# Performance work log

Hardware: AMD Instinct MI355X
Metric: run time of the kernel (lower is better)

Reference implementation:

```python
import jax, jax.numpy as jnp
import numpy as np

LMAX = 3
L2 = (LMAX + 1) ** 2
EPS = 1e-5
N_NODES = 2048
C_IN = 384
C_HID = 256


def _gaunt_tensor(lmax):
    # Real Gaunt coefficients G[i,j,k] = integral Y_i Y_j Y_k dOmega over S^2,
    # computed exactly with Gauss-Legendre (theta) x uniform (phi) quadrature.
    nt = 4 * lmax + 4
    nph = 8 * lmax + 8
    xg, wg = np.polynomial.legendre.leggauss(nt)
    ct, st = xg, np.sqrt(1.0 - xg ** 2)
    phi = 2.0 * np.pi * np.arange(nph) / nph
    # fully-normalized associated Legendre Pbar[l,m] on theta nodes
    P = np.zeros((lmax + 1, lmax + 1, nt))
    P[0, 0] = np.sqrt(1.0 / (4.0 * np.pi))
    for m in range(1, lmax + 1):
        P[m, m] = np.sqrt((2.0 * m + 1.0) / (2.0 * m)) * st * P[m - 1, m - 1]
    for m in range(lmax + 1):
        if m + 1 <= lmax:
            P[m + 1, m] = np.sqrt(2.0 * m + 3.0) * ct * P[m, m]
        for l in range(m + 2, lmax + 1):
            a = np.sqrt((4.0 * l * l - 1.0) / (l * l - m * m))
            b = np.sqrt(((l - 1.0) ** 2 - m * m) / (4.0 * (l - 1.0) ** 2 - 1.0))
            P[l, m] = a * (ct * P[l - 1, m] - b * P[l - 2, m])
    Y = np.zeros(((lmax + 1) ** 2, nt, nph))
    for l in range(lmax + 1):
        for m in range(-l, l + 1):
            idx = l * l + l + m
            if m == 0:
                Y[idx] = P[l, 0][:, None] * np.ones((1, nph))
            elif m > 0:
                Y[idx] = np.sqrt(2.0) * P[l, m][:, None] * np.cos(m * phi)[None, :]
            else:
                Y[idx] = np.sqrt(2.0) * P[l, -m][:, None] * np.sin(-m * phi)[None, :]
    W = wg[:, None] * (2.0 * np.pi / nph)  # [nt, nph]
    G = np.einsum('iap,jap,kap->ijk', Y, Y, Y * W[None])
    G[np.abs(G) < 1e-10] = 0.0
    return G


G_NP = _gaunt_tensor(LMAX)
SL = [slice(l * l, (l + 1) * (l + 1)) for l in range(LMAX + 1)]
_raw = []
for _l1 in range(LMAX + 1):
    for _l2 in range(LMAX + 1):
        for _l3 in range(LMAX + 1):
            _blk = G_NP[SL[_l1], SL[_l2], SL[_l3]]
            if np.abs(_blk).max() > 1e-8:
                _raw.append((_l1, _l2, _l3, _blk))
_fanin = {}
for _l1, _l2, _l3, _b in _raw:
    _fanin[_l3] = _fanin.get(_l3, 0) + 1
# component irrep normalization (sqrt(2l3+1)) and path normalization (1/sqrt(fan-in))
PATHS = [(l1, l2, l3, jnp.asarray((blk * np.sqrt(2.0 * l3 + 1.0) / np.sqrt(_fanin[l3])).astype(np.float32)))
         for (l1, l2, l3, blk) in _raw]
L_OF = jnp.asarray(np.repeat(np.arange(LMAX + 1), 2 * np.arange(LMAX + 1) + 1))  # [L2]


def setup_inputs() -> dict:
    key = jax.random.key(0)
    ks = jax.random.split(key, 9)
    inputs = jax.random.normal(ks[0], (N_NODES, L2, C_IN), jnp.float32)
    batch = jnp.sort(jax.random.randint(ks[1], (N_NODES,), 0, 64))
    norm_w = 1.0 + 0.1 * jax.random.normal(ks[2], (LMAX + 1, C_IN), jnp.float32)
    norm_b = 0.02 * jax.random.normal(ks[3], (C_IN,), jnp.float32)
    w1 = jax.random.normal(ks[4], (LMAX + 1, C_IN, C_HID), jnp.float32) / np.sqrt(C_IN)
    b1 = 0.02 * jax.random.normal(ks[5], (C_HID,), jnp.float32)
    w_gaunt = jax.random.normal(ks[6], (LMAX + 1, LMAX + 1, LMAX + 1, C_HID), jnp.float32)
    w2 = jax.random.normal(ks[7], (LMAX + 1, C_HID, C_IN), jnp.float32) / np.sqrt(C_HID)
    b2 = 0.02 * jax.random.normal(ks[8], (C_IN,), jnp.float32)
    return {"inputs": inputs, "batch": batch, "norm_w": norm_w, "norm_b": norm_b,
            "w1": w1, "b1": b1, "w_gaunt": w_gaunt, "w2": w2, "b2": b2}


def _forward(inputs, norm_w, norm_b, w1, b1, w_gaunt, w2, b2):
    # equivariant merge layer norm: center l=0 over channels, RMS over all (lm, C),
    # per-degree affine weight, bias on the l=0 (invariant) component only
    x = inputs
    x = x.at[:, 0, :].add(-jnp.mean(x[:, 0, :], axis=-1, keepdims=True))
    x = x * jax.lax.rsqrt(jnp.mean(x * x, axis=(1, 2), keepdims=True) + EPS)
    x = x * norm_w[L_OF][None]          # [N, L2, C]
    x = x.at[:, 0, :].add(norm_b)
    # SO3Linear 1: per-degree channel mixing, bias on l=0
    h = jnp.einsum('nic,ich->nih', x, w1[L_OF])
    h = h.at[:, 0, :].add(b1)
    # Gaunt depthwise self tensor product: per-channel CG-structured contraction
    t = jnp.zeros((inputs.shape[0], L2, w1.shape[-1]), dtype=h.dtype)
    for (l1, l2, l3, blk) in PATHS:
        hw = h[:, SL[l2], :] * w_gaunt[l1, l2, l3][None, None, :]     # [N, 2l2+1, H]
        tmp = jnp.einsum('ijk,nih->njkh', blk, h[:, SL[l1], :])       # small block contraction
        t = t.at[:, SL[l3], :].add(jnp.einsum('njkh,njh->nkh', tmp, hw))
    # SO3Linear 2
    out = jnp.einsum('nih,iho->nio', t, w2[L_OF])
    out = out.at[:, 0, :].add(b2)
    return out + inputs  # ffn_shortcut is Identity (num_in == num_out)


def reference(inputs, batch, norm_w, norm_b, w1, b1, w_gaunt, w2, b2):
    # drop_path / proj_drop are disabled (rates = 0); `batch` only feeds GraphDropPath
    return _forward(inputs, norm_w, norm_b, w1, b1, w_gaunt, w2, b2)
```

## Files before the change

kernel.cpp:

```cpp
#include <hip/hip_runtime.h>
#include <stdint.h>
#include <math.h>
#include <array>
#include <utility>

#ifndef M_PI
#define M_PI 3.14159265358979323846
#endif

#define NNODES 2048
#define L2DIM  16
#define CIN    384
#define CHID   256

typedef __attribute__((ext_vector_type(8))) short short8;
typedef __attribute__((ext_vector_type(4))) float f32x4;
typedef unsigned short u16;
typedef unsigned int   u32;

#define LOF(i) ((i) < 1 ? 0 : ((i) < 4 ? 1 : ((i) < 9 ? 2 : 3)))

static __device__ __forceinline__ u16 f2bf(float f) {
  u32 u = __builtin_bit_cast(u32, f);
  u = u + 0x7FFFu + ((u >> 16) & 1u);
  return (u16)(u >> 16);
}
static __device__ __forceinline__ float bf2f(u16 b) {
  u32 u = ((u32)b) << 16;
  return __builtin_bit_cast(float, u);
}

constexpr double CPI = 3.14159265358979323846;

constexpr double csqrt(double x) {
  if (x <= 0.0) return 0.0;
  double y = x > 1.0 ? x : 1.0;
  for (int i = 0; i < 48; ++i) y = 0.5 * (y + x / y);
  return y;
}
constexpr double ccos(double x) {
  double r = x;
  while (r > CPI)  r -= 2.0 * CPI;
  while (r < -CPI) r += 2.0 * CPI;
  double r2 = r * r, term = 1.0, sum = 1.0;
  for (int i = 1; i <= 26; ++i) { term *= -r2 / ((2.0 * i - 1.0) * (2.0 * i)); sum += term; }
  return sum;
}
constexpr int iabs_c(int x) { return x < 0 ? -x : x; }

struct GLQ { double x[16]; double w[16]; };
constexpr GLQ build_gl() {
  GLQ g{};
  const int n = 16;
  for (int i = 0; i < n; ++i) {
    double x = ccos(CPI * (i + 0.75) / (n + 0.5));
    double p1 = 0.0, dp = 1.0;
    for (int it = 0; it < 40; ++it) {
      double p0 = 1.0; p1 = x;
      for (int k = 2; k <= n; ++k) { double p2 = ((2.0*k-1.0)*x*p1 - (k-1.0)*p0)/k; p0 = p1; p1 = p2; }
      dp = n * (x*p1 - p0) / (x*x - 1.0);
      x -= p1 / dp;
    }
    { double p0 = 1.0; p1 = x;
      for (int k = 2; k <= n; ++k) { double p2 = ((2.0*k-1.0)*x*p1 - (k-1.0)*p0)/k; p0 = p1; p1 = p2; }
      dp = n * (x*p1 - p0) / (x*x - 1.0); }
    g.x[i] = x;
    g.w[i] = 2.0 / ((1.0 - x*x) * dp * dp);
  }
  return g;
}
constexpr GLQ QG = build_gl();

struct PTab { double v[4][4][16]; };
constexpr PTab build_pbar() {
  PTab T{};
  for (int t = 0; t < 16; ++t) {
    double ct = QG.x[t];
    double st = csqrt(1.0 - ct * ct);
    double P[4][4] = {};
    P[0][0] = csqrt(1.0 / (4.0 * CPI));
    for (int m = 1; m <= 3; ++m)
      P[m][m] = csqrt((2.0*m + 1.0) / (2.0*m)) * st * P[m-1][m-1];
    for (int m = 0; m <= 3; ++m) {
      if (m + 1 <= 3) P[m+1][m] = csqrt(2.0*m + 3.0) * ct * P[m][m];
      for (int l = m + 2; l <= 3; ++l) {
        double aa = csqrt((4.0*(double)l*l - 1.0) / ((double)l*l - (double)m*m));
        double bb = csqrt(((double)(l-1)*(l-1) - (double)m*m) / (4.0*(double)(l-1)*(l-1) - 1.0));
        P[l][m] = aa * (ct * P[l-1][m] - bb * P[l-2][m]);
      }
    }
    for (int l = 0; l < 4; ++l)
      for (int m = 0; m <= l; ++m) T.v[l][m][t] = P[l][m];
  }
  return T;
}
constexpr PTab PT = build_pbar();

constexpr double phi_int(int m1, int m2, int m3) {
  const double SQ2 = 1.41421356237309504880;
  int neg = (m1 < 0) + (m2 < 0) + (m3 < 0);
  if (neg & 1) return 0.0;
  int a = iabs_c(m1), b = iabs_c(m2), c = iabs_c(m3);
  int nz = (a > 0) + (b > 0) + (c > 0);
  if (nz == 0) return 2.0 * CPI;
  if (nz == 1) return 0.0;
  if (nz == 2) {
    int p = 0, q = 0;
    if (a == 0) { p = b; q = c; } else if (b == 0) { p = a; q = c; } else { p = a; q = b; }
    return (p == q) ? 2.0 * CPI : 0.0;
  }
  if (neg == 0) {
    double v = 0.0;
    if (iabs_c(a - b) == c && a != b) v += 1.0;
    if (a + b == c) v += 1.0;
    return SQ2 * CPI * v;
  }
  int p, q, r;
  if (m1 > 0)      { p = a; q = b; r = c; }
  else if (m2 > 0) { p = b; q = a; r = c; }
  else             { p = c; q = a; r = b; }
  double v = 0.0;
  if (q != r && p == iabs_c(q - r)) v += 1.0;
  if (p == q + r) v -= 1.0;
  return SQ2 * CPI * v;
}

constexpr bool path_ok(int l1, int l2, int l3) {
  int lo = l1 > l2 ? l1 - l2 : l2 - l1;
  return l3 >= lo && l3 <= l1 + l2 && (((l1 + l2 + l3) & 1) == 0);
}
constexpr bool term_ok(int m1, int m2, int m3) {
  int aa = iabs_c(m1), bb = iabs_c(m2), cc = iabs_c(m3);
  int neg = (m1 < 0) + (m2 < 0) + (m3 < 0);
  if (neg & 1) return false;
  return (aa + bb == cc) || (bb + cc == aa) || (cc + aa == bb);
}
constexpr int count_paths() {
  int n = 0;
  for (int l1 = 0; l1 < 4; ++l1) for (int l2 = 0; l2 < 4; ++l2) for (int l3 = 0; l3 < 4; ++l3)
    if (path_ok(l1, l2, l3)) ++n;
  return n;
}
constexpr int NPATHS = count_paths();
constexpr int NTMAX  = 512;

constexpr double term_g(int l1, int m1, int l2, int m2, int l3, int m3) {
  double ph = phi_int(m1, m2, m3);
  if (ph == 0.0) return 0.0;
  int a = iabs_c(m1), b = iabs_c(m2), c = iabs_c(m3);
  double s = 0.0;
  for (int t = 0; t < 16; ++t)
    s += QG.w[t] * PT.v[l1][a][t] * PT.v[l2][b][t] * PT.v[l3][c][t];
  double g = ph * s;
  double fan = (l3 == 0) ? 4.0 : (l3 == 1 ? 6.0 : (l3 == 2 ? 7.0 : 6.0));
  return g * csqrt((2.0 * (double)l3 + 1.0) / fan);
}

struct TermG { float g; unsigned char i, j, k, p; };
struct PathT { unsigned char l1, l2, l3; };
struct TGAll { TermG t[NTMAX]; int n; };
constexpr TGAll build_all() {
  TGAll r{};
  r.n = 0;
  int p = 0;
  for (int l1 = 0; l1 < 4; ++l1) for (int l2 = 0; l2 < 4; ++l2) for (int l3 = 0; l3 < 4; ++l3) {
    if (!path_ok(l1, l2, l3)) continue;
    for (int m1 = -l1; m1 <= l1; ++m1) for (int m2 = -l2; m2 <= l2; ++m2) for (int m3 = -l3; m3 <= l3; ++m3) {
      if (!term_ok(m1, m2, m3)) continue;
      double g = term_g(l1, m1, l2, m2, l3, m3);
      if (g > 1e-10 || g < -1e-10) {
        r.t[r.n].g = (float)g;
        r.t[r.n].i = (unsigned char)(l1 * l1 + l1 + m1);
        r.t[r.n].j = (unsigned char)(l2 * l2 + l2 + m2);
        r.t[r.n].k = (unsigned char)(l3 * l3 + l3 + m3);
        r.t[r.n].p = (unsigned char)p;
        ++r.n;
      }
    }
    ++p;
  }
  return r;
}
constexpr TGAll TGA = build_all();
constexpr int NNZ = TGA.n;

constexpr std::array<PathT, NPATHS> build_paths() {
  std::array<PathT, NPATHS> a{};
  int n = 0;
  for (int l1 = 0; l1 < 4; ++l1) for (int l2 = 0; l2 < 4; ++l2) for (int l3 = 0; l3 < 4; ++l3)
    if (path_ok(l1, l2, l3)) a[n++] = PathT{(unsigned char)l1, (unsigned char)l2, (unsigned char)l3};
  return a;
}
constexpr auto PATHS_ARR = build_paths();

template <size_t... Is>
__device__ __forceinline__ void gaunt_terms(std::index_sequence<Is...>,
    float* __restrict__ t, const float* __restrict__ h,
    const float* __restrict__ wgv) {
  ((t[TGA.t[Is].k] = fmaf(TGA.t[Is].g * wgv[TGA.t[Is].p],
                          h[TGA.t[Is].i] * h[TGA.t[Is].j],
                          t[TGA.t[Is].k])), ...);
}
template <size_t... Ps>
__device__ __forceinline__ void load_wgv(std::index_sequence<Ps...>,
    float* __restrict__ wgv, const float* __restrict__ wg, int c) {
  ((wgv[Ps] = wg[(size_t)(((int)PATHS_ARR[Ps].l1 * 4 + (int)PATHS_ARR[Ps].l2) * 4
                          + (int)PATHS_ARR[Ps].l3) * CHID + c]), ...);
}

__global__ __launch_bounds__(256) void transpose_bf16_kernel(
    const float* __restrict__ src, u16* __restrict__ dst, int R, int C) {
  __shared__ float tile[32][33];
  int mat = blockIdx.z;
  int r0 = blockIdx.y * 32, c0 = blockIdx.x * 32;
  const float* s = src + (size_t)mat * R * C;
  u16* d = dst + (size_t)mat * R * C;
  int tx = threadIdx.x & 31, ty = threadIdx.x >> 5;
  for (int rr = ty; rr < 32; rr += 8)
    tile[rr][tx] = s[(size_t)(r0 + rr) * C + (c0 + tx)];
  __syncthreads();
  for (int cc = ty; cc < 32; cc += 8)
    d[(size_t)(c0 + cc) * R + (r0 + tx)] = f2bf(tile[tx][cc]);
}

__global__ __launch_bounds__(256) void norm_kernel(
    const float* __restrict__ x, const float* __restrict__ nw,
    const float* __restrict__ nb, u16* __restrict__ xnb) {
  int n = blockIdx.x, tid = threadIdx.x;
  const float* xr = x + (size_t)n * (L2DIM * CIN);
  __shared__ float xs[L2DIM * CIN];
  __shared__ float2 red[4];
  float4 v[6];
  float ssq = 0.f;
#pragma unroll
  for (int q = 0; q < 6; ++q) {
    v[q] = reinterpret_cast<const float4*>(xr)[tid * 6 + q];
    ssq += v[q].x*v[q].x + v[q].y*v[q].y + v[q].z*v[q].z + v[q].w*v[q].w;
    reinterpret_cast<float4*>(xs)[tid * 6 + q] = v[q];
  }
  __syncthreads();
  float m0p = 0.f;
  for (int c = tid; c < CIN; c += 256) m0p += xs[c];
  float a = m0p, b = ssq;
#pragma unroll
  for (int off = 32; off > 0; off >>= 1) { a += __shfl_down(a, off, 64); b += __shfl_down(b, off, 64); }
  int lane = tid & 63, wid = tid >> 6;
  if (lane == 0) red[wid] = make_float2(a, b);
  __syncthreads();
  float sum0 = red[0].x + red[1].x + red[2].x + red[3].x;
  float ssqt = red[0].y + red[1].y + red[2].y + red[3].y;
  float mean0 = sum0 * (1.0f / CIN);
  float ss = ssqt - (float)CIN * mean0 * mean0;
  float rstd = rsqrtf(ss * (1.0f / (L2DIM * CIN)) + 1e-5f);

  int lm = tid >> 4;
  int l = LOF(lm);
  bool row0 = (lm == 0);
  int cbase = (tid & 15) * 24;
  u16* orow = xnb + (size_t)n * (L2DIM * CIN) + (size_t)tid * 24;
#pragma unroll
  for (int q = 0; q < 6; ++q) {
    int c = cbase + q * 4;
    float4 w4 = *reinterpret_cast<const float4*>(&nw[l * CIN + c]);
    float4 b4 = row0 ? *reinterpret_cast<const float4*>(&nb[c]) : make_float4(0,0,0,0);
    float sub = row0 ? mean0 : 0.f;
    float o0 = (v[q].x - sub) * rstd * w4.x + b4.x;
    float o1 = (v[q].y - sub) * rstd * w4.y + b4.y;
    float o2 = (v[q].z - sub) * rstd * w4.z + b4.z;
    float o3 = (v[q].w - sub) * rstd * w4.w + b4.w;
    ushort4 pk;
    pk.x = f2bf(o0); pk.y = f2bf(o1); pk.z = f2bf(o2); pk.w = f2bf(o3);
    *reinterpret_cast<ushort4*>(&orow[q * 4]) = pk;
  }
}

template <int KD, int ND, bool SECOND>
__global__ __launch_bounds__(256) void so3_gemm_kernel(
    const u16* __restrict__ A, const u16* __restrict__ BT,
    const float* __restrict__ bias, const float* __restrict__ resid,
    u16* __restrict__ outb, float* __restrict__ outf) {
  int l = blockIdx.z;
  int twol1 = 2 * l + 1;
  int mtiles = (NNODES * twol1) >> 6;
  if ((int)blockIdx.x >= mtiles) return;
  int col0 = blockIdx.y * 128;
  int tid = threadIdx.x, lane = tid & 63, wid = tid >> 6;
  int wm = wid >> 1, wn = wid & 1;

  __shared__ u16 Asm[64 * 64];
  __shared__ u16 Bsm[128 * 64];

  const u16* asrc[2];
#pragma unroll
  for (int rr = 0; rr < 2; ++rr) {
    int r = wid * 16 + rr * 8 + (lane >> 3);
    int Rg = blockIdx.x * 64 + r;
    int node = Rg / twol1;
    int lm = l * l + (Rg - node * twol1);
    asrc[rr] = A + (size_t)(node * L2DIM + lm) * KD + ((lane & 7) ^ (r & 7)) * 8;
  }
  const u16* bsrc[4];
#pragma unroll
  for (int rr = 0; rr < 4; ++rr) {
    int r = wid * 32 + rr * 8 + (lane >> 3);
    int colg = col0 + r;
    bsrc[rr] = BT + (size_t)(l * ND + colg) * KD + ((lane & 7) ^ (r & 7)) * 8;
  }

  f32x4 acc[2][4];
#pragma unroll
  for (int i = 0; i < 2; ++i)
#pragma unroll
    for (int j = 0; j < 4; ++j) acc[i][j] = (f32x4){0.f, 0.f, 0.f, 0.f};

  for (int kt = 0; kt < KD / 64; ++kt) {
#pragma unroll
    for (int rr = 0; rr < 2; ++rr)
      __builtin_amdgcn_global_load_lds(
          (const __attribute__((address_space(1))) void*)(asrc[rr] + kt * 64),
          (__attribute__((address_space(3))) void*)(&Asm[wid * 1024 + rr * 512]),
          16, 0, 0);
#pragma unroll
    for (int rr = 0; rr < 4; ++rr)
      __builtin_amdgcn_global_load_lds(
          (const __attribute__((address_space(1))) void*)(bsrc[rr] + kt * 64),
          (__attribute__((address_space(3))) void*)(&Bsm[wid * 2048 + rr * 512]),
          16, 0, 0);
    __syncthreads();
#pragma unroll
    for (int ks = 0; ks < 2; ++ks) {
      short8 af[2], bfv[4];
#pragma unroll
      for (int mf = 0; mf < 2; ++mf) {
        int row = wm * 32 + mf * 16 + (lane & 15);
        int slot = (ks * 4 + (lane >> 4)) ^ (row & 7);
        af[mf] = *reinterpret_cast<const short8*>(&Asm[row * 64 + slot * 8]);
      }
#pragma unroll
      for (int nf = 0; nf < 4; ++nf) {
        int brow = wn * 64 + nf * 16 + (lane & 15);
        int slot = (ks * 4 + (lane >> 4)) ^ (brow & 7);
        bfv[nf] = *reinterpret_cast<const short8*>(&Bsm[brow * 64 + slot * 8]);
      }
#pragma unroll
      for (int mf = 0; mf < 2; ++mf)
#pragma unroll
        for (int nf = 0; nf < 4; ++nf)
          acc[mf][nf] = __builtin_amdgcn_mfma_f32_16x16x32_bf16(af[mf], bfv[nf], acc[mf][nf], 0, 0, 0);
    }
    __syncthreads();
  }

#pragma unroll
  for (int mf = 0; mf < 2; ++mf) {
#pragma unroll
    for (int jj = 0; jj < 4; ++jj) {
      int Rg = blockIdx.x * 64 + wm * 32 + mf * 16 + (lane >> 4) * 4 + jj;
      int node = Rg / twol1;
      int lm = l * l + (Rg - node * twol1);
      size_t rowoff = (size_t)(node * L2DIM + lm);
#pragma unroll
      for (int nf = 0; nf < 4; ++nf) {
        int colg = col0 + wn * 64 + nf * 16 + (lane & 15);
        float vv = acc[mf][nf][jj];
        if (l == 0) vv += bias[colg];
        if (!SECOND) {
          outb[rowoff * ND + colg] = f2bf(vv);
        } else {
          outf[rowoff * ND + colg] = vv + resid[rowoff * ND + colg];
        }
      }
    }
  }
}

__global__ __launch_bounds__(256, 2) void gaunt_kernel(
    const u16* __restrict__ hb, const float* __restrict__ wg,
    u16* __restrict__ tb) {
  int n = blockIdx.x, c = threadIdx.x;
  const u16* hr = hb + (size_t)n * (L2DIM * CHID) + c;
  float h[16];
#pragma unroll
  for (int i = 0; i < 16; ++i) h[i] = bf2f(hr[i * CHID]);

  float wgv[NPATHS];
  load_wgv(std::make_index_sequence<NPATHS>{}, wgv, wg, c);

  float t[16];
#pragma unroll
  for (int k = 0; k < 16; ++k) t[k] = 0.f;

  gaunt_terms(std::make_index_sequence<NNZ>{}, t, h, wgv);

  u16* tr = tb + (size_t)n * (L2DIM * CHID) + c;
#pragma unroll
  for (int k = 0; k < 16; ++k) tr[k * CHID] = f2bf(t[k]);
}

extern "C" void kernel_launch(void* const* d_in, const int* in_sizes, int n_in,
                              void* d_out, int out_size, void* d_ws, size_t ws_size,
                              hipStream_t stream) {
  const float* inputs = (const float*)d_in[0];
  const float* norm_w = (const float*)d_in[2];
  const float* norm_b = (const float*)d_in[3];
  const float* w1     = (const float*)d_in[4];
  const float* b1     = (const float*)d_in[5];
  const float* wga    = (const float*)d_in[6];
  const float* w2     = (const float*)d_in[7];
  const float* b2     = (const float*)d_in[8];
  float* out = (float*)d_out;

  uint8_t* ws = (uint8_t*)d_ws;
  u16*   w1t = (u16*)(ws + 16384);
  u16*   w2t = (u16*)(ws + 802816);
  u16*   xnb = (u16*)(ws + 1589248);
  u16*   tb  = xnb;
  u16*   hb  = (u16*)(ws + 26755072);

  transpose_bf16_kernel<<<dim3(8, 12, 4), 256, 0, stream>>>(w1, w1t, 384, 256);
  transpose_bf16_kernel<<<dim3(12, 8, 4), 256, 0, stream>>>(w2, w2t, 256, 384);
  norm_kernel<<<NNODES, 256, 0, stream>>>(inputs, norm_w, norm_b, xnb);
  so3_gemm_kernel<CIN, CHID, false><<<dim3(224, 2, 4), 256, 0, stream>>>(
      xnb, w1t, b1, nullptr, hb, nullptr);
  gaunt_kernel<<<NNODES, 256, 0, stream>>>(hb, wga, tb);
  so3_gemm_kernel<CHID, CIN, true><<<dim3(224, 3, 4), 256, 0, stream>>>(
      tb, w2t, b2, inputs, nullptr, out);
}
```

Before: 93.13 us.

## Widen GEMM tiles to full N, merge transposes, drop LDS staging in norm

Each SO3 GEMM block now covers the whole output width (256 or 384 columns) with 512 threads and 8 waves, instead of 128-column tiles. The A tile is therefore loaded once per row block rather than once per column tile, and fewer blocks are launched. The two weight-transpose launches are merged into one grid that returns early for out-of-range tiles. The norm kernel computes the l=0 mean from registers rather than staging the whole row in shared memory, which removes a large LDS buffer and a barrier. In exchange, each GEMM block uses more LDS and more accumulator registers, and fewer blocks are available to spread across the CUs.

```diff
diff --git a/kernel.cpp b/kernel.cpp
--- a/kernel.cpp
+++ b/kernel.cpp
@@ -115,7 +115,7 @@
     if (a + b == c) v += 1.0;
     return SQ2 * CPI * v;
   }
-  int p, q, r;
+  int p = 0, q = 0, r = 0;
   if (m1 > 0)      { p = a; q = b; r = c; }
   else if (m2 > 0) { p = b; q = a; r = c; }
   else             { p = c; q = a; r = b; }
@@ -209,12 +209,15 @@
 }
 
 __global__ __launch_bounds__(256) void transpose_bf16_kernel(
-    const float* __restrict__ src, u16* __restrict__ dst, int R, int C) {
+    const float* __restrict__ w1, const float* __restrict__ w2,
+    u16* __restrict__ w1t, u16* __restrict__ w2t) {
   __shared__ float tile[32][33];
-  int mat = blockIdx.z;
+  int z = blockIdx.z;
+  int R = z < 4 ? 384 : 256, C = z < 4 ? 256 : 384;
   int r0 = blockIdx.y * 32, c0 = blockIdx.x * 32;
-  const float* s = src + (size_t)mat * R * C;
-  u16* d = dst + (size_t)mat * R * C;
+  if (r0 >= R || c0 >= C) return;
+  const float* s = (z < 4 ? w1 : w2) + (size_t)(z & 3) * R * C;
+  u16* d = (z < 4 ? w1t : w2t) + (size_t)(z & 3) * R * C;
   int tx = threadIdx.x & 31, ty = threadIdx.x >> 5;
   for (int rr = ty; rr < 32; rr += 8)
     tile[rr][tx] = s[(size_t)(r0 + rr) * C + (c0 + tx)];
@@ -228,19 +231,18 @@
     const float* __restrict__ nb, u16* __restrict__ xnb) {
   int n = blockIdx.x, tid = threadIdx.x;
   const float* xr = x + (size_t)n * (L2DIM * CIN);
-  __shared__ float xs[L2DIM * CIN];
   __shared__ float2 red[4];
   float4 v[6];
-  float ssq = 0.f;
+  float ssq = 0.f, m0p = 0.f;
 #pragma unroll
   for (int q = 0; q < 6; ++q) {
     v[q] = reinterpret_cast<const float4*>(xr)[tid * 6 + q];
     ssq += v[q].x*v[q].x + v[q].y*v[q].y + v[q].z*v[q].z + v[q].w*v[q].w;
-    reinterpret_cast<float4*>(xs)[tid * 6 + q] = v[q];
-  }
-  __syncthreads();
-  float m0p = 0.f;
-  for (int c = tid; c < CIN; c += 256) m0p += xs[c];
+  }
+  if (tid < 16) {
+#pragma unroll
+    for (int q = 0; q < 6; ++q) m0p += v[q].x + v[q].y + v[q].z + v[q].w;
+  }
   float a = m0p, b = ssq;
 #pragma unroll
   for (int off = 32; off > 0; off >>= 1) { a += __shfl_down(a, off, 64); b += __shfl_down(b, off, 64); }
@@ -275,61 +277,59 @@
 }
 
 template <int KD, int ND, bool SECOND>
-__global__ __launch_bounds__(256) void so3_gemm_kernel(
+__global__ __launch_bounds__(512) void so3_gemm_kernel(
     const u16* __restrict__ A, const u16* __restrict__ BT,
     const float* __restrict__ bias, const float* __restrict__ resid,
     u16* __restrict__ outb, float* __restrict__ outf) {
+  constexpr int NFRAG = ND / 64;
+  constexpr int WN_T = ND / 4;
+  static_assert((ND % 64) == 0 && NFRAG * 16 == WN_T, "");
   int l = blockIdx.z;
   int twol1 = 2 * l + 1;
   int mtiles = (NNODES * twol1) >> 6;
   if ((int)blockIdx.x >= mtiles) return;
-  int col0 = blockIdx.y * 128;
   int tid = threadIdx.x, lane = tid & 63, wid = tid >> 6;
-  int wm = wid >> 1, wn = wid & 1;
+  int wm = wid >> 2, wn = wid & 3;
 
   __shared__ u16 Asm[64 * 64];
-  __shared__ u16 Bsm[128 * 64];
-
-  const u16* asrc[2];
-#pragma unroll
-  for (int rr = 0; rr < 2; ++rr) {
-    int r = wid * 16 + rr * 8 + (lane >> 3);
-    int Rg = blockIdx.x * 64 + r;
+  __shared__ u16 Bsm[ND * 64];
+
+  int ar = tid >> 3;
+  const u16* asrc;
+  {
+    int Rg = blockIdx.x * 64 + ar;
     int node = Rg / twol1;
     int lm = l * l + (Rg - node * twol1);
-    asrc[rr] = A + (size_t)(node * L2DIM + lm) * KD + ((lane & 7) ^ (r & 7)) * 8;
-  }
-  const u16* bsrc[4];
-#pragma unroll
-  for (int rr = 0; rr < 4; ++rr) {
-    int r = wid * 32 + rr * 8 + (lane >> 3);
-    int colg = col0 + r;
-    bsrc[rr] = BT + (size_t)(l * ND + colg) * KD + ((lane & 7) ^ (r & 7)) * 8;
-  }
-
-  f32x4 acc[2][4];
+    asrc = A + (size_t)(node * L2DIM + lm) * KD + ((tid & 7) ^ (ar & 7)) * 8;
+  }
+  const u16* bsrc[ND / 64];
+#pragma unroll
+  for (int i = 0; i < ND / 64; ++i) {
+    int r = i * 64 + (tid >> 3);
+    bsrc[i] = BT + (size_t)(l * ND + r) * KD + ((tid & 7) ^ (r & 7)) * 8;
+  }
+
+  f32x4 acc[2][NFRAG];
 #pragma unroll
   for (int i = 0; i < 2; ++i)
 #pragma unroll
-    for (int j = 0; j < 4; ++j) acc[i][j] = (f32x4){0.f, 0.f, 0.f, 0.f};
+    for (int j = 0; j < NFRAG; ++j) acc[i][j] = (f32x4){0.f, 0.f, 0.f, 0.f};
 
   for (int kt = 0; kt < KD / 64; ++kt) {
-#pragma unroll
-    for (int rr = 0; rr < 2; ++rr)
+    __builtin_amdgcn_global_load_lds(
+        (const __attribute__((address_space(1))) void*)(asrc + kt * 64),
+        (__attribute__((address_space(3))) void*)(&Asm[wid * 512]),
+        16, 0, 0);
+#pragma unroll
+    for (int i = 0; i < ND / 64; ++i)
       __builtin_amdgcn_global_load_lds(
-          (const __attribute__((address_space(1))) void*)(asrc[rr] + kt * 64),
-          (__attribute__((address_space(3))) void*)(&Asm[wid * 1024 + rr * 512]),
-          16, 0, 0);
-#pragma unroll
-    for (int rr = 0; rr < 4; ++rr)
-      __builtin_amdgcn_global_load_lds(
-          (const __attribute__((address_space(1))) void*)(bsrc[rr] + kt * 64),
-          (__attribute__((address_space(3))) void*)(&Bsm[wid * 2048 + rr * 512]),
+          (const __attribute__((address_space(1))) void*)(bsrc[i] + kt * 64),
+          (__attribute__((address_space(3))) void*)(&Bsm[i * 4096 + wid * 512]),
           16, 0, 0);
     __syncthreads();
 #pragma unroll
     for (int ks = 0; ks < 2; ++ks) {
-      short8 af[2], bfv[4];
+      short8 af[2], bfv[NFRAG];
 #pragma unroll
       for (int mf = 0; mf < 2; ++mf) {
         int row = wm * 32 + mf * 16 + (lane & 15);
@@ -337,15 +337,15 @@
         af[mf] = *reinterpret_cast<const short8*>(&Asm[row * 64 + slot * 8]);
       }
 #pragma unroll
-      for (int nf = 0; nf < 4; ++nf) {
-        int brow = wn * 64 + nf * 16 + (lane & 15);
+      for (int nf = 0; nf < NFRAG; ++nf) {
+        int brow = wn * WN_T + nf * 16 + (lane & 15);
         int slot = (ks * 4 + (lane >> 4)) ^ (brow & 7);
         bfv[nf] = *reinterpret_cast<const short8*>(&Bsm[brow * 64 + slot * 8]);
       }
 #pragma unroll
       for (int mf = 0; mf < 2; ++mf)
 #pragma unroll
-        for (int nf = 0; nf < 4; ++nf)
+        for (int nf = 0; nf < NFRAG; ++nf)
           acc[mf][nf] = __builtin_amdgcn_mfma_f32_16x16x32_bf16(af[mf], bfv[nf], acc[mf][nf], 0, 0, 0);
     }
     __syncthreads();
@@ -360,8 +360,8 @@
       int lm = l * l + (Rg - node * twol1);
       size_t rowoff = (size_t)(node * L2DIM + lm);
 #pragma unroll
-      for (int nf = 0; nf < 4; ++nf) {
-        int colg = col0 + wn * 64 + nf * 16 + (lane & 15);
+      for (int nf = 0; nf < NFRAG; ++nf) {
+        int colg = wn * WN_T + nf * 16 + (lane & 15);
         float vv = acc[mf][nf][jj];
         if (l == 0) vv += bias[colg];
         if (!SECOND) {
@@ -417,12 +417,11 @@
   u16*   tb  = xnb;
   u16*   hb  = (u16*)(ws + 26755072);
 
-  transpose_bf16_kernel<<<dim3(8, 12, 4), 256, 0, stream>>>(w1, w1t, 384, 256);
-  transpose_bf16_kernel<<<dim3(12, 8, 4), 256, 0, stream>>>(w2, w2t, 256, 384);
+  transpose_bf16_kernel<<<dim3(12, 12, 8), 256, 0, stream>>>(w1, w2, w1t, w2t);
   norm_kernel<<<NNODES, 256, 0, stream>>>(inputs, norm_w, norm_b, xnb);
-  so3_gemm_kernel<CIN, CHID, false><<<dim3(224, 2, 4), 256, 0, stream>>>(
+  so3_gemm_kernel<CIN, CHID, false><<<dim3(224, 1, 4), 512, 0, stream>>>(
       xnb, w1t, b1, nullptr, hb, nullptr);
   gaunt_kernel<<<NNODES, 256, 0, stream>>>(hb, wga, tb);
-  so3_gemm_kernel<CHID, CIN, true><<<dim3(224, 3, 4), 256, 0, stream>>>(
+  so3_gemm_kernel<CHID, CIN, true><<<dim3(224, 1, 4), 512, 0, stream>>>(
       tb, w2t, b2, inputs, nullptr, out);
 }
```

Result: no change. 92.14 us (-1.1%).
